# Kernel optimization log

Measured on AMD Instinct MI355X. Metric: run time of the kernel, lower is better.

The kernel has to match this reference:

```python
import jax, jax.numpy as jnp
import numpy as np

N = 100000      # num_nodes
E = 1600000     # num_edges (avg degree 16)
EMB = 128       # emb_dim
HID = 128       # hidden_size
REPR = 64       # repr_dim


def setup_inputs() -> dict:
    key = jax.random.key(0)
    k0, k1, k2, k3 = jax.random.split(key, 4)
    edge_index = jax.random.randint(k0, (2, E), 0, N)
    node_emb = jax.random.normal(k1, (N, EMB), jnp.float32) * 0.1
    # GCNConv weights: glorot-like init, bias zeros (PyG default)
    W1 = jax.random.normal(k2, (EMB, HID), jnp.float32) * (1.0 / np.sqrt(EMB))
    b1 = jnp.zeros((HID,), jnp.float32)
    W2 = jax.random.normal(k3, (HID, REPR), jnp.float32) * (1.0 / np.sqrt(HID))
    b2 = jnp.zeros((REPR,), jnp.float32)
    return {"edge_index": edge_index, "node_emb": node_emb,
            "W1": W1, "b1": b1, "W2": W2, "b2": b2}


def reference(edge_index, node_emb, W1, b1, W2, b2):
    # PyG GCNConv: add self-loops, symmetric degree normalization,
    # out = scatter_add(norm * (x W)[src] -> dst) + b
    loops = jnp.arange(N, dtype=edge_index.dtype)
    src = jnp.concatenate([edge_index[0], loops])  # [E+N]
    dst = jnp.concatenate([edge_index[1], loops])
    deg = jax.ops.segment_sum(jnp.ones_like(src, dtype=node_emb.dtype), dst,
                              num_segments=N)
    dinv = jax.lax.rsqrt(deg)  # deg >= 1 thanks to self-loops
    norm = dinv[src] * dinv[dst]  # [E+N]

    def gcn_conv(x, W, b):
        h = x @ W                                   # [N, out]
        msg = norm[:, None] * h[src]                # gather + scale, [E+N, out]
        return jax.ops.segment_sum(msg, dst, num_segments=N) + b

    x = jax.nn.relu(gcn_conv(node_emb, W1, b1))
    # F.dropout(training=False) is identity in eval mode
    return gcn_conv(x, W2, b2)
```

## Files before the change

### kernel.cpp

```cpp
#include <hip/hip_runtime.h>
#include <hip/hip_bf16.h>
#include <stdint.h>


static constexpr int KD = 128;
static constexpr int BSH = 8;
static constexpr int MAXB = 512;
static constexpr int CHUNK = 2048;
static constexpr int CAP = 6144;

typedef short bf16x8 __attribute__((ext_vector_type(8)));
typedef float f32x4  __attribute__((ext_vector_type(4)));
typedef float f32x2  __attribute__((ext_vector_type(2)));

__device__ __forceinline__ unsigned short f2bf(float f) {
    __hip_bfloat16 b = __float2bfloat16(f);
    return *reinterpret_cast<unsigned short*>(&b);
}
__device__ __forceinline__ float bflo(unsigned v) { return __uint_as_float(v << 16); }
__device__ __forceinline__ float bfhi(unsigned v) { return __uint_as_float(v & 0xffff0000u); }
__device__ __forceinline__ unsigned pk2(float lo, float hi) {
    return (unsigned)f2bf(lo) | ((unsigned)f2bf(hi) << 16);
}
__device__ __forceinline__ void accp(f32x2* a, uint4 v) {
    f32x2 t;
    t.x = bflo(v.x); t.y = bfhi(v.x); a[0] += t;
    t.x = bflo(v.y); t.y = bfhi(v.y); a[1] += t;
    t.x = bflo(v.z); t.y = bfhi(v.z); a[2] += t;
    t.x = bflo(v.w); t.y = bfhi(v.w); a[3] += t;
}

__global__ __launch_bounds__(256) void init_hist(const float* __restrict__ W1,
        const float* __restrict__ W2, unsigned short* __restrict__ Wt1,
        unsigned short* __restrict__ Wt2, const int* __restrict__ dst,
        int* __restrict__ ghist, int e, int nbuck) {
    __shared__ int cnt[MAXB];
    const int t = threadIdx.x;
    const int e0 = blockIdx.x * CHUNK;
    const int m = min(CHUNK, e - e0);
    for (int i = t; i < nbuck; i += 256) cnt[i] = 0;
    __syncthreads();
    for (int i = t; i < m; i += 256) atomicAdd(&cnt[dst[e0 + i] >> BSH], 1);
    int g = blockIdx.x * 256 + t;
    if (g < 128 * 128) {
        int k = g >> 7, nn = g & 127;
        Wt1[nn * 128 + k] = f2bf(W1[g]);
    } else if (g < 128 * 128 + 128 * 64) {
        int i = g - 128 * 128;
        int k = i >> 6, nn = i & 63;
        Wt2[nn * 128 + k] = f2bf(W2[i]);
    }
    __syncthreads();
    for (int i = t; i < nbuck; i += 256) ghist[blockIdx.x * nbuck + i] = cnt[i];
}

__global__ __launch_bounds__(256) void chunk_scan(int* __restrict__ ghist,
        int* __restrict__ bcur, int nchunk, int nbuck) {
    __shared__ int wsum[4];
    const int t = threadIdx.x;
    const int b = blockIdx.x;
    const int lane = t & 63, wv = t >> 6;
    int carry = 0;
    for (int t0 = 0; t0 < nchunk; t0 += 256) {
        int c = t0 + t;
        int v = (c < nchunk) ? ghist[c * nbuck + b] : 0;
        int iv = v;
        for (int off = 1; off < 64; off <<= 1) {
            int u = __shfl_up(iv, off, 64);
            if (lane >= off) iv += u;
        }
        if (lane == 63) wsum[wv] = iv;
        __syncthreads();
        int woff = 0;
        for (int i = 0; i < wv; ++i) woff += wsum[i];
        int total = wsum[0] + wsum[1] + wsum[2] + wsum[3];
        int excl = iv - v + woff;
        if (c < nchunk) ghist[c * nbuck + b] = b * CAP + carry + excl;
        carry += total;
        __syncthreads();
    }
    if (t == 0) bcur[b] = b * CAP + carry;
}

__global__ __launch_bounds__(256) void chunk_scatter(const int* __restrict__ src,
        const int* __restrict__ dst, const int* __restrict__ ghist,
        int* __restrict__ packed, int e, int nbuck) {
    __shared__ int cur[MAXB];
    const int t = threadIdx.x;
    const int e0 = blockIdx.x * CHUNK;
    const int m = min(CHUNK, e - e0);
    for (int i = t; i < nbuck; i += 256) cur[i] = ghist[blockIdx.x * nbuck + i];
    __syncthreads();
    for (int i = t; i < m; i += 256) {
        int d = dst[e0 + i], s = src[e0 + i];
        int b = d >> BSH;
        int p = atomicAdd(&cur[b], 1);
        if (p < (b + 1) * CAP)
            packed[p] = ((d & ((1 << BSH) - 1)) << 24) | s;
    }
}

__global__ __launch_bounds__(256) void bucket_build(const int* __restrict__ packed,
        const int* __restrict__ bcur, int* __restrict__ roff, int* __restrict__ degN,
        float* __restrict__ dinv, int* __restrict__ csr, int n) {
    __shared__ int deg[1 << BSH];
    __shared__ int cur[1 << BSH];
    __shared__ int wsum[4];
    const int t = threadIdx.x;
    const int b = blockIdx.x;
    const int nodeBase = b << BSH;
    const int nn = min(1 << BSH, n - nodeBase);
    const int e0 = b * CAP, e1 = bcur[b];

    deg[t] = 0;
    __syncthreads();
    for (int i = e0 + t; i < e1; i += 256)
        atomicAdd(&deg[(unsigned)packed[i] >> 24], 1);
    __syncthreads();

    const int d = deg[t];
    int lane = t & 63, wv = t >> 6;
    int iv = d;
    for (int off = 1; off < 64; off <<= 1) {
        int u = __shfl_up(iv, off, 64);
        if (lane >= off) iv += u;
    }
    if (lane == 63) wsum[wv] = iv;
    __syncthreads();
    int woff = 0;
    for (int i = 0; i < wv; ++i) woff += wsum[i];
    int excl = iv - d + woff;
    cur[t] = excl;
    if (t < nn) {
        roff[nodeBase + t] = e0 + excl;
        degN[nodeBase + t] = d;
        dinv[nodeBase + t] = rsqrtf((float)(d + 1));
    }
    __syncthreads();

    for (int i = e0 + t; i < e1; i += 256) {
        unsigned pk = (unsigned)packed[i];
        int dl = pk >> 24;
        int s = pk & 0xFFFFFF;
        int slot = atomicAdd(&cur[dl], 1);
        csr[e0 + slot] = s;
    }
}

template<int C, bool XBF>
__global__ __launch_bounds__(256) void gemm_mfma(const void* __restrict__ xv,
        const unsigned short* __restrict__ Wt, const float* __restrict__ dinv,
        unsigned short* __restrict__ out, int n)
{
    constexpr int KP = KD + 8;
    constexpr int WP = 64 + 8;
    __shared__ __align__(16) unsigned short xt[64 * KP];
    __shared__ __align__(16) unsigned short lw[C * WP];
    const int t = threadIdx.x;
    const int w = t >> 6, lane = t & 63;
    const int quad = lane >> 4, l16 = lane & 15;
    const int row0 = blockIdx.x * 64;

    for (int i = t; i < 64 * 32; i += 256) {
        int r = i >> 5, c4 = (i & 31) * 4;
        int row = row0 + r;
        ushort4 pk = make_ushort4(0, 0, 0, 0);
        if (row < n) {
            if constexpr (XBF) {
                pk = *reinterpret_cast<const ushort4*>(
                    &((const unsigned short*)xv)[(size_t)row * KD + c4]);
            } else {
                float4 v = *reinterpret_cast<const float4*>(
                    &((const float*)xv)[(size_t)row * KD + c4]);
                pk.x = f2bf(v.x); pk.y = f2bf(v.y); pk.z = f2bf(v.z); pk.w = f2bf(v.w);
            }
        }
        *reinterpret_cast<ushort4*>(&xt[r * KP + c4]) = pk;
    }

    f32x4 acc[C / 16];
#pragma unroll
    for (int i = 0; i < C / 16; ++i) acc[i] = (f32x4)(0.f);

    for (int h = 0; h < 2; ++h) {
        __syncthreads();
        for (int i = t; i < C * 16; i += 256) {
            int nr = i >> 4, j = (i & 15) * 4;
            *reinterpret_cast<ushort4*>(&lw[nr * WP + j]) =
                *reinterpret_cast<const ushort4*>(&Wt[nr * KD + h * 64 + j]);
        }
        __syncthreads();
#pragma unroll
        for (int kt = 0; kt < 2; ++kt) {
            bf16x8 af = *reinterpret_cast<const bf16x8*>(
                &xt[(w * 16 + l16) * KP + h * 64 + kt * 32 + quad * 8]);
#pragma unroll
            for (int ct = 0; ct < C / 16; ++ct) {
                bf16x8 bfr = *reinterpret_cast<const bf16x8*>(
                    &lw[(ct * 16 + l16) * WP + kt * 32 + quad * 8]);
                acc[ct] = __builtin_amdgcn_mfma_f32_16x16x32_bf16(af, bfr, acc[ct], 0, 0, 0);
            }
        }
    }

#pragma unroll
    for (int j = 0; j < 4; ++j) {
        int row = row0 + w * 16 + quad * 4 + j;
        if (row < n) {
            float s = dinv[row];
#pragma unroll
            for (int ct = 0; ct < C / 16; ++ct)
                out[(size_t)row * C + ct * 16 + l16] = f2bf(acc[ct][j] * s);
        }
    }
}

__global__ __launch_bounds__(256) void gather128(const uint4* __restrict__ H,
        const int* __restrict__ roff, const int* __restrict__ degN,
        const int* __restrict__ csr, const float* __restrict__ dinv,
        const float* __restrict__ b, uint4* __restrict__ out, int n)
{
    int wid = (blockIdx.x * 256 + threadIdx.x) >> 6;
    int lane = threadIdx.x & 63;
    if (wid >= n) return;
    const int qw = lane >> 4, cp = lane & 15;
    const char* Hb = (const char*)H;
    const unsigned cpo = (unsigned)cp * 16u;
    f32x2 a[4], c[4];
#pragma unroll
    for (int i = 0; i < 4; ++i) { a[i] = (f32x2)(0.f); c[i] = (f32x2)(0.f); }
    int e0 = roff[wid], e1 = e0 + degN[wid];
    for (int base = e0; base < e1; base += 64) {
        int m = e1 - base; if (m > 64) m = 64;
        int idx = (lane < m) ? csr[base + lane] : 0;
        int j = 0;
        for (; j + 8 <= m; j += 8) {
            unsigned u0 = (unsigned)__shfl(idx, j + qw);
            unsigned u1 = (unsigned)__shfl(idx, j + 4 + qw);
            uint4 v0 = *(const uint4*)(Hb + ((u0 << 8) + cpo));
            uint4 v1 = *(const uint4*)(Hb + ((u1 << 8) + cpo));
            accp(a, v0);
            accp(c, v1);
        }
        for (; j + 4 <= m; j += 4) {
            unsigned u = (unsigned)__shfl(idx, j + qw);
            uint4 v = *(const uint4*)(Hb + ((u << 8) + cpo));
            accp(a, v);
        }
        int r = m - j;
        if (r) {
            unsigned u = (unsigned)__shfl(idx, min(j + qw, m - 1));
            if (qw < r) {
                uint4 v = *(const uint4*)(Hb + ((u << 8) + cpo));
                accp(a, v);
            }
        }
    }
#pragma unroll
    for (int i = 0; i < 4; ++i) a[i] += c[i];
#pragma unroll
    for (int i = 0; i < 4; ++i) {
        a[i].x += __shfl_xor(a[i].x, 16, 64);
        a[i].x += __shfl_xor(a[i].x, 32, 64);
        a[i].y += __shfl_xor(a[i].y, 16, 64);
        a[i].y += __shfl_xor(a[i].y, 32, 64);
    }
    if (qw == 0) {
        uint4 sv = *(const uint4*)(Hb + (((unsigned)wid << 8) + cpo));
        accp(a, sv);
        float s = dinv[wid];
        float4 b0 = ((const float4*)b)[cp * 2];
        float4 b1 = ((const float4*)b)[cp * 2 + 1];
        float r0 = fmaxf(s * a[0].x + b0.x, 0.f), r1 = fmaxf(s * a[0].y + b0.y, 0.f);
        float r2 = fmaxf(s * a[1].x + b0.z, 0.f), r3 = fmaxf(s * a[1].y + b0.w, 0.f);
        float r4 = fmaxf(s * a[2].x + b1.x, 0.f), r5 = fmaxf(s * a[2].y + b1.y, 0.f);
        float r6 = fmaxf(s * a[3].x + b1.z, 0.f), r7 = fmaxf(s * a[3].y + b1.w, 0.f);
        uint4 o;
        o.x = pk2(r0, r1); o.y = pk2(r2, r3); o.z = pk2(r4, r5); o.w = pk2(r6, r7);
        out[(size_t)wid * 16 + cp] = o;
    }
}

__global__ __launch_bounds__(256) void gather64(const uint4* __restrict__ H,
        const int* __restrict__ roff, const int* __restrict__ degN,
        const int* __restrict__ csr, const float* __restrict__ dinv,
        const float* __restrict__ b, float4* __restrict__ out, int n)
{
    int wpair = (blockIdx.x * 256 + threadIdx.x) >> 6;
    int lane = threadIdx.x & 63;
    const int half = lane >> 5, h32 = half << 5;
    const int oc = (lane >> 3) & 3, cp = lane & 7;
    const int l32 = lane & 31;
    const int node = wpair * 2 + half;
    const char* Hb = (const char*)H;
    const unsigned cpo = (unsigned)cp * 16u;
    f32x2 a[4], c[4];
#pragma unroll
    for (int i = 0; i < 4; ++i) { a[i] = (f32x2)(0.f); c[i] = (f32x2)(0.f); }
    int e0 = 0, deg = 0;
    if (node < n) { e0 = roff[node]; deg = degN[node]; }
    for (int base = 0; base < deg; base += 32) {
        int m = deg - base; if (m > 32) m = 32;
        int idx = (l32 < m) ? csr[e0 + base + l32] : 0;
        int j = 0;
        for (; j + 8 <= m; j += 8) {
            unsigned u0 = (unsigned)__shfl(idx, h32 + j + oc, 64);
            unsigned u1 = (unsigned)__shfl(idx, h32 + j + 4 + oc, 64);
            uint4 v0 = *(const uint4*)(Hb + ((u0 << 7) + cpo));
            uint4 v1 = *(const uint4*)(Hb + ((u1 << 7) + cpo));
            accp(a, v0);
            accp(c, v1);
        }
        for (; j + 4 <= m; j += 4) {
            unsigned u = (unsigned)__shfl(idx, h32 + j + oc, 64);
            uint4 v = *(const uint4*)(Hb + ((u << 7) + cpo));
            accp(a, v);
        }
        int r = m - j;
        if (r) {
            unsigned u = (unsigned)__shfl(idx, h32 + min(j + oc, m - 1), 64);
            if (oc < r) {
                uint4 v = *(const uint4*)(Hb + ((u << 7) + cpo));
                accp(a, v);
            }
        }
    }
#pragma unroll
    for (int i = 0; i < 4; ++i) a[i] += c[i];
#pragma unroll
    for (int i = 0; i < 4; ++i) {
        a[i].x += __shfl_xor(a[i].x, 8, 64);
        a[i].x += __shfl_xor(a[i].x, 16, 64);
        a[i].y += __shfl_xor(a[i].y, 8, 64);
        a[i].y += __shfl_xor(a[i].y, 16, 64);
    }
    if (oc == 0 && node < n) {
        uint4 sv = *(const uint4*)(Hb + (((unsigned)node << 7) + cpo));
        accp(a, sv);
        float s = dinv[node];
        float4 b0 = ((const float4*)b)[cp * 2];
        float4 b1 = ((const float4*)b)[cp * 2 + 1];
        float4 o0 = make_float4(s * a[0].x + b0.x, s * a[0].y + b0.y,
                                s * a[1].x + b0.z, s * a[1].y + b0.w);
        float4 o1 = make_float4(s * a[2].x + b1.x, s * a[2].y + b1.y,
                                s * a[3].x + b1.z, s * a[3].y + b1.w);
        out[(size_t)node * 16 + cp * 2] = o0;
        out[(size_t)node * 16 + cp * 2 + 1] = o1;
    }
}

extern "C" void kernel_launch(void* const* d_in, const int* in_sizes, int n_in,
                              void* d_out, int out_size, void* d_ws, size_t ws_size,
                              hipStream_t stream)
{
    const int* ei = (const int*)d_in[0];
    const int E = in_sizes[0] / 2;
    const float* emb = (const float*)d_in[1];
    const int N = in_sizes[1] / KD;
    const float* W1 = (const float*)d_in[2];
    const float* b1 = (const float*)d_in[3];
    const float* W2 = (const float*)d_in[4];
    const float* b2 = (const float*)d_in[5];
    const int* src = ei;
    const int* dst = ei + E;
    const int nbuck = (N + (1 << BSH) - 1) >> BSH;
    const int nchunk = (E + CHUNK - 1) / CHUNK;

    char* p = (char*)d_ws;
    auto alloc = [&](size_t bytes) { char* q = p; p += (bytes + 255) & ~(size_t)255; return q; };
    unsigned short* h1 = (unsigned short*)alloc((size_t)N * 128 * sizeof(unsigned short));
    unsigned short* x2 = (unsigned short*)alloc((size_t)N * 128 * sizeof(unsigned short));
    int*   csr    = (int*)  alloc((size_t)nbuck * CAP * sizeof(int));
    int*   packed = (int*)  alloc((size_t)nbuck * CAP * sizeof(int));
    int*   ghist  = (int*)  alloc((size_t)nchunk * nbuck * sizeof(int));
    int*   roff   = (int*)  alloc((size_t)N * sizeof(int));
    int*   degN   = (int*)  alloc((size_t)N * sizeof(int));
    float* dinv   = (float*)alloc((size_t)N * sizeof(float));
    int*   bcur   = (int*)  alloc(MAXB * sizeof(int));
    unsigned short* Wt1 = (unsigned short*)alloc(128 * 128 * sizeof(unsigned short));
    unsigned short* Wt2 = (unsigned short*)alloc(64 * 128 * sizeof(unsigned short));
    unsigned short* h2 = h1;

    init_hist<<<nchunk, 256, 0, stream>>>(W1, W2, Wt1, Wt2, dst, ghist, E, nbuck);
    chunk_scan<<<nbuck, 256, 0, stream>>>(ghist, bcur, nchunk, nbuck);
    chunk_scatter<<<nchunk, 256, 0, stream>>>(src, dst, ghist, packed, E, nbuck);
    bucket_build<<<nbuck, 256, 0, stream>>>(packed, bcur, roff, degN, dinv, csr, N);

    gemm_mfma<128, false><<<(N + 63) / 64, 256, 0, stream>>>(emb, Wt1, dinv, h1, N);
    gather128<<<(N + 3) / 4, 256, 0, stream>>>((const uint4*)h1, roff, degN, csr,
                                               dinv, b1, (uint4*)x2, N);

    gemm_mfma<64, true><<<(N + 63) / 64, 256, 0, stream>>>(x2, Wt2, dinv, h2, N);
    gather64<<<(N + 7) / 8, 256, 0, stream>>>((const uint4*)h2, roff, degN, csr,
                                              dinv, b2, (float4*)d_out, N);
}
```

Before: 286.9 us.

## Fuse first GEMM into edge-scatter launch and narrow gather64 to quarter-wave nodes

The layer-1 GEMM no longer needs dinv, so it is launched in the same grid as the edge scatter (extra blocks do GEMM), overlapping graph preprocessing with matmul and removing one launch. To compensate, gather128 now scales each neighbor row by dinv[src] on the fly, which adds a scattered dinv load per edge. gather64 is reworked to process four nodes per wave with 16-lane groups instead of two nodes with 32-lane groups, reducing wasted lanes for low-degree nodes and one shuffle-reduction stage. The fused kernel carries the GEMM's shared memory for scatter blocks too, which may lower occupancy.

Measured after the change: 280.1 us, median of 2. 2.3% less time.

```diff
diff --git a/kernel.cpp b/kernel.cpp
--- a/kernel.cpp
+++ b/kernel.cpp
@@ -28,6 +28,14 @@
     t.x = bflo(v.y); t.y = bfhi(v.y); a[1] += t;
     t.x = bflo(v.z); t.y = bfhi(v.z); a[2] += t;
     t.x = bflo(v.w); t.y = bfhi(v.w); a[3] += t;
+}
+__device__ __forceinline__ void accf(f32x2* a, uint4 v, float d) {
+    f32x2 dd; dd.x = d; dd.y = d;
+    f32x2 t;
+    t.x = bflo(v.x); t.y = bfhi(v.x); a[0] += dd * t;
+    t.x = bflo(v.y); t.y = bfhi(v.y); a[1] += dd * t;
+    t.x = bflo(v.z); t.y = bfhi(v.z); a[2] += dd * t;
+    t.x = bflo(v.w); t.y = bfhi(v.w); a[3] += dd * t;
 }
 
 __global__ __launch_bounds__(256) void init_hist(const float* __restrict__ W1,
@@ -82,21 +90,82 @@
     if (t == 0) bcur[b] = b * CAP + carry;
 }
 
-__global__ __launch_bounds__(256) void chunk_scatter(const int* __restrict__ src,
+__global__ __launch_bounds__(256) void scatter_gemm(const int* __restrict__ src,
         const int* __restrict__ dst, const int* __restrict__ ghist,
-        int* __restrict__ packed, int e, int nbuck) {
+        int* __restrict__ packed, int e, int nbuck, int nscatter,
+        const float* __restrict__ xv, const unsigned short* __restrict__ Wt,
+        unsigned short* __restrict__ out, int n)
+{
+    constexpr int C = 128;
+    constexpr int KP = KD + 8;
+    constexpr int WP = 64 + 8;
+    __shared__ __align__(16) unsigned short xt[64 * KP];
+    __shared__ __align__(16) unsigned short lw[C * WP];
     __shared__ int cur[MAXB];
     const int t = threadIdx.x;
-    const int e0 = blockIdx.x * CHUNK;
-    const int m = min(CHUNK, e - e0);
-    for (int i = t; i < nbuck; i += 256) cur[i] = ghist[blockIdx.x * nbuck + i];
-    __syncthreads();
-    for (int i = t; i < m; i += 256) {
-        int d = dst[e0 + i], s = src[e0 + i];
-        int b = d >> BSH;
-        int p = atomicAdd(&cur[b], 1);
-        if (p < (b + 1) * CAP)
-            packed[p] = ((d & ((1 << BSH) - 1)) << 24) | s;
+
+    if (blockIdx.x < nscatter) {
+        const int e0 = blockIdx.x * CHUNK;
+        const int m = min(CHUNK, e - e0);
+        for (int i = t; i < nbuck; i += 256) cur[i] = ghist[blockIdx.x * nbuck + i];
+        __syncthreads();
+        for (int i = t; i < m; i += 256) {
+            int d = dst[e0 + i], s = src[e0 + i];
+            int b = d >> BSH;
+            int p = atomicAdd(&cur[b], 1);
+            if (p < (b + 1) * CAP)
+                packed[p] = ((d & ((1 << BSH) - 1)) << 24) | s;
+        }
+        return;
+    }
+
+    const int w = t >> 6, lane = t & 63;
+    const int quad = lane >> 4, l16 = lane & 15;
+    const int row0 = (blockIdx.x - nscatter) * 64;
+
+    for (int i = t; i < 64 * 32; i += 256) {
+        int r = i >> 5, c4 = (i & 31) * 4;
+        int row = row0 + r;
+        ushort4 pk = make_ushort4(0, 0, 0, 0);
+        if (row < n) {
+            float4 v = *reinterpret_cast<const float4*>(&xv[(size_t)row * KD + c4]);
+            pk.x = f2bf(v.x); pk.y = f2bf(v.y); pk.z = f2bf(v.z); pk.w = f2bf(v.w);
+        }
+        *reinterpret_cast<ushort4*>(&xt[r * KP + c4]) = pk;
+    }
+
+    f32x4 acc[C / 16];
+#pragma unroll
+    for (int i = 0; i < C / 16; ++i) acc[i] = (f32x4)(0.f);
+
+    for (int h = 0; h < 2; ++h) {
+        __syncthreads();
+        for (int i = t; i < C * 16; i += 256) {
+            int nr = i >> 4, j = (i & 15) * 4;
+            *reinterpret_cast<ushort4*>(&lw[nr * WP + j]) =
+                *reinterpret_cast<const ushort4*>(&Wt[nr * KD + h * 64 + j]);
+        }
+        __syncthreads();
+#pragma unroll
+        for (int kt = 0; kt < 2; ++kt) {
+            bf16x8 af = *reinterpret_cast<const bf16x8*>(
+                &xt[(w * 16 + l16) * KP + h * 64 + kt * 32 + quad * 8]);
+#pragma unroll
+            for (int ct = 0; ct < C / 16; ++ct) {
+                bf16x8 bfr = *reinterpret_cast<const bf16x8*>(
+                    &lw[(ct * 16 + l16) * WP + kt * 32 + quad * 8]);
+                acc[ct] = __builtin_amdgcn_mfma_f32_16x16x32_bf16(af, bfr, acc[ct], 0, 0, 0);
+            }
+        }
+    }
+#pragma unroll
+    for (int j = 0; j < 4; ++j) {
+        int row = row0 + w * 16 + quad * 4 + j;
+        if (row < n) {
+#pragma unroll
+            for (int ct = 0; ct < C / 16; ++ct)
+                out[(size_t)row * C + ct * 16 + l16] = f2bf(acc[ct][j]);
+        }
     }
 }
 
@@ -147,11 +216,11 @@
     }
 }
 
-template<int C, bool XBF>
-__global__ __launch_bounds__(256) void gemm_mfma(const void* __restrict__ xv,
+__global__ __launch_bounds__(256) void gemm_mfma64(const unsigned short* __restrict__ xv,
         const unsigned short* __restrict__ Wt, const float* __restrict__ dinv,
         unsigned short* __restrict__ out, int n)
 {
+    constexpr int C = 64;
     constexpr int KP = KD + 8;
     constexpr int WP = 64 + 8;
     __shared__ __align__(16) unsigned short xt[64 * KP];
@@ -165,16 +234,8 @@
         int r = i >> 5, c4 = (i & 31) * 4;
         int row = row0 + r;
         ushort4 pk = make_ushort4(0, 0, 0, 0);
-        if (row < n) {
-            if constexpr (XBF) {
-                pk = *reinterpret_cast<const ushort4*>(
-                    &((const unsigned short*)xv)[(size_t)row * KD + c4]);
-            } else {
-                float4 v = *reinterpret_cast<const float4*>(
-                    &((const float*)xv)[(size_t)row * KD + c4]);
-                pk.x = f2bf(v.x); pk.y = f2bf(v.y); pk.z = f2bf(v.z); pk.w = f2bf(v.w);
-            }
-        }
+        if (row < n)
+            pk = *reinterpret_cast<const ushort4*>(&xv[(size_t)row * KD + c4]);
         *reinterpret_cast<ushort4*>(&xt[r * KP + c4]) = pk;
     }
 
@@ -202,7 +263,6 @@
             }
         }
     }
-
 #pragma unroll
     for (int j = 0; j < 4; ++j) {
         int row = row0 + w * 16 + quad * 4 + j;
@@ -237,22 +297,25 @@
         for (; j + 8 <= m; j += 8) {
             unsigned u0 = (unsigned)__shfl(idx, j + qw);
             unsigned u1 = (unsigned)__shfl(idx, j + 4 + qw);
+            float d0 = dinv[u0], d1 = dinv[u1];
             uint4 v0 = *(const uint4*)(Hb + ((u0 << 8) + cpo));
             uint4 v1 = *(const uint4*)(Hb + ((u1 << 8) + cpo));
-            accp(a, v0);
-            accp(c, v1);
+            accf(a, v0, d0);
+            accf(c, v1, d1);
         }
         for (; j + 4 <= m; j += 4) {
             unsigned u = (unsigned)__shfl(idx, j + qw);
+            float d0 = dinv[u];
             uint4 v = *(const uint4*)(Hb + ((u << 8) + cpo));
-            accp(a, v);
+            accf(a, v, d0);
         }
         int r = m - j;
         if (r) {
             unsigned u = (unsigned)__shfl(idx, min(j + qw, m - 1));
             if (qw < r) {
+                float d0 = dinv[u];
                 uint4 v = *(const uint4*)(Hb + ((u << 8) + cpo));
-                accp(a, v);
+                accf(a, v, d0);
             }
         }
     }
@@ -266,9 +329,9 @@
         a[i].y += __shfl_xor(a[i].y, 32, 64);
     }
     if (qw == 0) {
+        float s = dinv[wid];
         uint4 sv = *(const uint4*)(Hb + (((unsigned)wid << 8) + cpo));
-        accp(a, sv);
-        float s = dinv[wid];
+        accf(a, sv, s);
         float4 b0 = ((const float4*)b)[cp * 2];
         float4 b1 = ((const float4*)b)[cp * 2 + 1];
         float r0 = fmaxf(s * a[0].x + b0.x, 0.f), r1 = fmaxf(s * a[0].y + b0.y, 0.f);
@@ -286,12 +349,12 @@
         const int* __restrict__ csr, const float* __restrict__ dinv,
         const float* __restrict__ b, float4* __restrict__ out, int n)
 {
-    int wpair = (blockIdx.x * 256 + threadIdx.x) >> 6;
+    int wquad = (blockIdx.x * 256 + threadIdx.x) >> 6;
     int lane = threadIdx.x & 63;
-    const int half = lane >> 5, h32 = half << 5;
-    const int oc = (lane >> 3) & 3, cp = lane & 7;
-    const int l32 = lane & 31;
-    const int node = wpair * 2 + half;
+    const int q16 = lane & 48;
+    const int l16 = lane & 15;
+    const int oc = l16 >> 3, cp = lane & 7;
+    const int node = wquad * 4 + (q16 >> 4);
     const char* Hb = (const char*)H;
     const unsigned cpo = (unsigned)cp * 16u;
     f32x2 a[4], c[4];
@@ -299,27 +362,26 @@
     for (int i = 0; i < 4; ++i) { a[i] = (f32x2)(0.f); c[i] = (f32x2)(0.f); }
     int e0 = 0, deg = 0;
     if (node < n) { e0 = roff[node]; deg = degN[node]; }
-    for (int base = 0; base < deg; base += 32) {
-        int m = deg - base; if (m > 32) m = 32;
-        int idx = (l32 < m) ? csr[e0 + base + l32] : 0;
+    for (int base = 0; base < deg; base += 16) {
+        int m = deg - base; if (m > 16) m = 16;
+        int idx = (l16 < m) ? csr[e0 + base + l16] : 0;
         int j = 0;
-        for (; j + 8 <= m; j += 8) {
-            unsigned u0 = (unsigned)__shfl(idx, h32 + j + oc, 64);
-            unsigned u1 = (unsigned)__shfl(idx, h32 + j + 4 + oc, 64);
+        for (; j + 4 <= m; j += 4) {
+            unsigned u0 = (unsigned)__shfl(idx, q16 + j + oc, 64);
+            unsigned u1 = (unsigned)__shfl(idx, q16 + j + 2 + oc, 64);
             uint4 v0 = *(const uint4*)(Hb + ((u0 << 7) + cpo));
             uint4 v1 = *(const uint4*)(Hb + ((u1 << 7) + cpo));
             accp(a, v0);
             accp(c, v1);
         }
-        for (; j + 4 <= m; j += 4) {
-            unsigned u = (unsigned)__shfl(idx, h32 + j + oc, 64);
+        for (; j + 2 <= m; j += 2) {
+            unsigned u = (unsigned)__shfl(idx, q16 + j + oc, 64);
             uint4 v = *(const uint4*)(Hb + ((u << 7) + cpo));
             accp(a, v);
         }
-        int r = m - j;
-        if (r) {
-            unsigned u = (unsigned)__shfl(idx, h32 + min(j + oc, m - 1), 64);
-            if (oc < r) {
+        if (j < m) {
+            unsigned u = (unsigned)__shfl(idx, q16 + m - 1, 64);
+            if (oc == 0) {
                 uint4 v = *(const uint4*)(Hb + ((u << 7) + cpo));
                 accp(a, v);
             }
@@ -330,9 +392,7 @@
 #pragma unroll
     for (int i = 0; i < 4; ++i) {
         a[i].x += __shfl_xor(a[i].x, 8, 64);
-        a[i].x += __shfl_xor(a[i].x, 16, 64);
         a[i].y += __shfl_xor(a[i].y, 8, 64);
-        a[i].y += __shfl_xor(a[i].y, 16, 64);
     }
     if (oc == 0 && node < n) {
         uint4 sv = *(const uint4*)(Hb + (((unsigned)node << 7) + cpo));
@@ -383,14 +443,15 @@
 
     init_hist<<<nchunk, 256, 0, stream>>>(W1, W2, Wt1, Wt2, dst, ghist, E, nbuck);
     chunk_scan<<<nbuck, 256, 0, stream>>>(ghist, bcur, nchunk, nbuck);
-    chunk_scatter<<<nchunk, 256, 0, stream>>>(src, dst, ghist, packed, E, nbuck);
+    const int ngemm1 = (N + 63) / 64;
+    scatter_gemm<<<nchunk + ngemm1, 256, 0, stream>>>(src, dst, ghist, packed, E,
+                                                      nbuck, nchunk, emb, Wt1, h1, N);
     bucket_build<<<nbuck, 256, 0, stream>>>(packed, bcur, roff, degN, dinv, csr, N);
 
-    gemm_mfma<128, false><<<(N + 63) / 64, 256, 0, stream>>>(emb, Wt1, dinv, h1, N);
     gather128<<<(N + 3) / 4, 256, 0, stream>>>((const uint4*)h1, roff, degN, csr,
                                                dinv, b1, (uint4*)x2, N);
 
-    gemm_mfma<64, true><<<(N + 63) / 64, 256, 0, stream>>>(x2, Wt2, dinv, h2, N);
-    gather64<<<(N + 7) / 8, 256, 0, stream>>>((const uint4*)h2, roff, degN, csr,
-                                              dinv, b2, (float4*)d_out, N);
-}
+    gemm_mfma64<<<(N + 63) / 64, 256, 0, stream>>>(x2, Wt2, dinv, h2, N);
+    gather64<<<(N + 15) / 16, 256, 0, stream>>>((const uint4*)h2, roff, degN, csr,
+                                                dinv, b2, (float4*)d_out, N);
+}
```
